# Performance work log

Hardware: AMD Instinct MI355X
Metric: run time of the kernel (lower is better)

## Reference

```python
import jax, jax.numpy as jnp
from jax import lax
import numpy as np

DIM = 8
C = 192
N = 198  # 2 special tokens + 14*14 patches (distilled=True)
B = 1024


def quick_gelu(x):
    return x * jax.nn.sigmoid(1.702 * x)


def setup_inputs() -> dict:
    key = jax.random.key(0)
    ks = jax.random.split(key, 7)
    return {
        "x": jax.random.normal(ks[0], (B, N, C), dtype=jnp.float32),
        "w_down": jax.random.normal(ks[1], (DIM, C), dtype=jnp.float32) * 0.05,
        "b_down": jnp.zeros((DIM,), dtype=jnp.float32),
        "conv_w": jax.random.normal(ks[2], (DIM, DIM, 3, 3), dtype=jnp.float32) * 0.05,
        "conv_b": jnp.zeros((DIM,), dtype=jnp.float32),
        "w_up": jax.random.normal(ks[3], (C, DIM), dtype=jnp.float32) * 0.05,
        "b_up": jnp.zeros((C,), dtype=jnp.float32),
    }


def _conv3x3(t, conv_w, conv_b):
    # t: [B, dim, H, W]; 3x3, stride 1, pad 1 (SAME)
    y = lax.conv_general_dilated(
        t, conv_w, window_strides=(1, 1), padding=((1, 1), (1, 1)),
        dimension_numbers=("NCHW", "OIHW", "NCHW"))
    return y + conv_b[None, :, None, None]


def reference(x, w_down, b_down, conv_w, conv_b, w_up, b_up):
    b, n, c = x.shape
    dim = w_down.shape[0]
    # down projection + QuickGELU
    d = quick_gelu(jnp.einsum("bnc,dc->bnd", x, w_down) + b_down)
    # patch tokens -> [B, dim, 14, 14] -> conv -> [B, 196, dim]
    x_patch = d[:, 2:].reshape(b, 14, 14, dim).transpose(0, 3, 1, 2)
    x_patch = _conv3x3(x_patch, conv_w, conv_b)
    x_patch = x_patch.transpose(0, 2, 3, 1).reshape(b, 14 * 14, dim)
    # cls token -> [B, dim, 1, 1] -> conv (only center tap contributes) -> [B, 1, dim]
    x_cls = d[:, :1].reshape(b, 1, 1, dim).transpose(0, 3, 1, 2)
    x_cls = _conv3x3(x_cls, conv_w, conv_b)
    x_cls = x_cls.transpose(0, 2, 3, 1).reshape(b, 1, dim)
    zero_dist = jnp.zeros_like(x_cls)
    d2 = jnp.concatenate([x_cls, zero_dist, x_patch], axis=1)
    d2 = quick_gelu(d2)  # dropout is identity in eval mode
    return jnp.einsum("bnd,cd->bnc", d2, w_up) + b_up
```

## Files before the change

### kernel.cpp

```cpp
#include <hip/hip_runtime.h>
#include <math.h>

#define NTOK 198
#define CCH  192
#define DIMV 8

typedef float vf4 __attribute__((ext_vector_type(4)));

__device__ __forceinline__ float qgelu(float v) {
    return v / (1.0f + __expf(-1.702f * v));
}

__global__ __launch_bounds__(512, 2) void convpass_fused(
    const float* __restrict__ x,
    const float* __restrict__ w_down,
    const float* __restrict__ b_down,
    const float* __restrict__ conv_w,
    const float* __restrict__ conv_b,
    const float* __restrict__ w_up,
    const float* __restrict__ b_up,
    float* __restrict__ out)
{
    const int b   = blockIdx.x;
    const int tid = threadIdx.x;

    __shared__ float s_w[8 * CCH];
    __shared__ float s_d[NTOK * 9];
    __shared__ float s_d2[NTOK * 8];
    __shared__ float s_cw[576];
    __shared__ float s_cb[8];

    for (int t = tid; t < 8 * CCH; t += 512) s_w[t] = w_down[t];
    for (int t = tid; t < 576; t += 512) {
        const int kk = t >> 6, rem = t & 63, i = rem >> 3, o = rem & 7;
        s_cw[t] = conv_w[(o * 8 + i) * 9 + kk];
    }
    if (tid < 8) s_cb[tid] = conv_b[tid];
    __syncthreads();

    {
        const int lane  = tid & 63;
        const int wv    = tid >> 6;
        const int t_sub = lane >> 3;
        const int k     = lane & 7;
        const float bd  = b_down[k];
        const float* xb = x + (size_t)b * NTOK * CCH;

        #pragma unroll 1
        for (int p = 0; p < 4; ++p) {
            const int n = p * 64 + wv * 8 + t_sub;
            const bool valid = (n < NTOK);
            const int nn = valid ? n : (NTOK - 1);
            const float* xr = xb + (size_t)nn * CCH + k * 24;

            float4 xa[6];
            #pragma unroll
            for (int j = 0; j < 6; ++j) xa[j] = *(const float4*)(xr + 4 * j);

            float acc[8] = {0,0,0,0,0,0,0,0};
            #pragma unroll
            for (int j = 0; j < 6; ++j) {
                #pragma unroll
                for (int dm = 0; dm < 8; ++dm) {
                    const float4 wv4 = *(const float4*)&s_w[dm * CCH + k * 24 + j * 4];
                    acc[dm] += xa[j].x * wv4.x + xa[j].y * wv4.y
                             + xa[j].z * wv4.z + xa[j].w * wv4.w;
                }
            }
            float outv = 0.f;
            #pragma unroll
            for (int dm = 0; dm < 8; ++dm) {
                float v = acc[dm];
                v += __shfl_xor(v, 1); v += __shfl_xor(v, 2); v += __shfl_xor(v, 4);
                outv = (dm == k) ? v : outv;
            }
            if (valid) s_d[n * 9 + k] = qgelu(outv + bd);
        }
    }
    __syncthreads();

    for (int j = tid; j < NTOK * 8; j += 512) {
        const int n = j >> 3, o = j & 7;
        if (n == 1) {
            s_d2[j] = 0.0f;
        } else if (n == 0) {
            float acc = s_cb[o];
            #pragma unroll
            for (int i = 0; i < 8; ++i)
                acc += s_d[i] * s_cw[4 * 64 + i * 8 + o];
            s_d2[j] = qgelu(acc);
        } else {
            const int pos = n - 2, h = pos / 14, w = pos % 14;
            float acc = s_cb[o];
            #pragma unroll
            for (int dh = -1; dh <= 1; ++dh) {
                const int hh = h + dh;
                if (hh < 0 || hh > 13) continue;
                #pragma unroll
                for (int dw = -1; dw <= 1; ++dw) {
                    const int ww = w + dw;
                    if (ww < 0 || ww > 13) continue;
                    const int tok = 2 + hh * 14 + ww;
                    const int kk  = (dh + 1) * 3 + (dw + 1);
                    #pragma unroll
                    for (int i = 0; i < 8; ++i)
                        acc += s_d[tok * 9 + i] * s_cw[kk * 64 + i * 8 + o];
                }
            }
            s_d2[j] = qgelu(acc);
        }
    }

    const int c4 = tid % 48;
    const int tl = tid / 48;
    float w_r[4][8];
    #pragma unroll
    for (int cc = 0; cc < 4; ++cc) {
        const float4 wa = *(const float4*)(w_up + (c4 * 4 + cc) * 8);
        const float4 wb = *(const float4*)(w_up + (c4 * 4 + cc) * 8 + 4);
        w_r[cc][0] = wa.x; w_r[cc][1] = wa.y; w_r[cc][2] = wa.z; w_r[cc][3] = wa.w;
        w_r[cc][4] = wb.x; w_r[cc][5] = wb.y; w_r[cc][6] = wb.z; w_r[cc][7] = wb.w;
    }
    const float4 bu = *(const float4*)(b_up + c4 * 4);
    __syncthreads();

    if (tl < 10) {
        float* outb = out + (size_t)b * NTOK * CCH;
        #pragma unroll 1
        for (int nr = tl; nr < NTOK; nr += 10) {
            const float4 da = *(const float4*)&s_d2[nr * 8];
            const float4 dv = *(const float4*)&s_d2[nr * 8 + 4];
            float accs[4] = {bu.x, bu.y, bu.z, bu.w};
            #pragma unroll
            for (int cc = 0; cc < 4; ++cc) {
                accs[cc] += da.x * w_r[cc][0] + da.y * w_r[cc][1]
                          + da.z * w_r[cc][2] + da.w * w_r[cc][3]
                          + dv.x * w_r[cc][4] + dv.y * w_r[cc][5]
                          + dv.z * w_r[cc][6] + dv.w * w_r[cc][7];
            }
            const vf4 r = {accs[0], accs[1], accs[2], accs[3]};
            __builtin_nontemporal_store(r, (vf4*)(outb + (size_t)nr * CCH + c4 * 4));
        }
    }
}

extern "C" void kernel_launch(void* const* d_in, const int* in_sizes, int n_in,
                              void* d_out, int out_size, void* d_ws, size_t ws_size,
                              hipStream_t stream) {
    const float* x      = (const float*)d_in[0];
    const float* w_down = (const float*)d_in[1];
    const float* b_down = (const float*)d_in[2];
    const float* conv_w = (const float*)d_in[3];
    const float* conv_b = (const float*)d_in[4];
    const float* w_up   = (const float*)d_in[5];
    const float* b_up   = (const float*)d_in[6];
    float* out = (float*)d_out;

    const int B = in_sizes[0] / (NTOK * CCH);
    convpass_fused<<<dim3(B), dim3(512), 0, stream>>>(
        x, w_down, b_down, conv_w, conv_b, w_up, b_up, out);
}
```

Before: 86.11 us.

## Double-buffer x row loads and use a recursive-halving shuffle reduction

```diff
diff --git a/kernel.cpp b/kernel.cpp
--- a/kernel.cpp
+++ b/kernel.cpp
@@ -45,18 +45,14 @@
         const int k     = lane & 7;
         const float bd  = b_down[k];
         const float* xb = x + (size_t)b * NTOK * CCH;
+        const int base  = wv * 8 + t_sub;
 
-        #pragma unroll 1
-        for (int p = 0; p < 4; ++p) {
-            const int n = p * 64 + wv * 8 + t_sub;
-            const bool valid = (n < NTOK);
-            const int nn = valid ? n : (NTOK - 1);
-            const float* xr = xb + (size_t)nn * CCH + k * 24;
+        auto rowp = [&](int n) {
+            const int nn = (n < NTOK) ? n : (NTOK - 1);
+            return xb + (size_t)nn * CCH + k * 24;
+        };
 
-            float4 xa[6];
-            #pragma unroll
-            for (int j = 0; j < 6; ++j) xa[j] = *(const float4*)(xr + 4 * j);
-
+        auto compute = [&](const float4* xa, int n) {
             float acc[8] = {0,0,0,0,0,0,0,0};
             #pragma unroll
             for (int j = 0; j < 6; ++j) {
@@ -67,15 +63,51 @@
                              + xa[j].z * wv4.z + xa[j].w * wv4.w;
                 }
             }
-            float outv = 0.f;
+            float r4[4];
             #pragma unroll
-            for (int dm = 0; dm < 8; ++dm) {
-                float v = acc[dm];
-                v += __shfl_xor(v, 1); v += __shfl_xor(v, 2); v += __shfl_xor(v, 4);
-                outv = (dm == k) ? v : outv;
+            for (int m = 0; m < 4; ++m) {
+                const float give = (k & 1) ? acc[2*m]     : acc[2*m + 1];
+                const float keep = (k & 1) ? acc[2*m + 1] : acc[2*m];
+                r4[m] = keep + __shfl_xor(give, 1);
             }
-            if (valid) s_d[n * 9 + k] = qgelu(outv + bd);
+            float r2[2];
+            #pragma unroll
+            for (int m = 0; m < 2; ++m) {
+                const float give = (k & 2) ? r4[2*m]     : r4[2*m + 1];
+                const float keep = (k & 2) ? r4[2*m + 1] : r4[2*m];
+                r2[m] = keep + __shfl_xor(give, 2);
+            }
+            const float give = (k & 4) ? r2[0] : r2[1];
+            const float keep = (k & 4) ? r2[1] : r2[0];
+            const float v = keep + __shfl_xor(give, 4);
+            if (n < NTOK) s_d[n * 9 + k] = qgelu(v + bd);
+        };
+
+        float4 bufA[6], bufB[6];
+        {
+            const float* p = rowp(base);
+            #pragma unroll
+            for (int j = 0; j < 6; ++j) bufA[j] = *(const float4*)(p + 4 * j);
         }
+        {
+            const float* p = rowp(base + 64);
+            #pragma unroll
+            for (int j = 0; j < 6; ++j) bufB[j] = *(const float4*)(p + 4 * j);
+        }
+        compute(bufA, base);
+        {
+            const float* p = rowp(base + 128);
+            #pragma unroll
+            for (int j = 0; j < 6; ++j) bufA[j] = *(const float4*)(p + 4 * j);
+        }
+        compute(bufB, base + 64);
+        {
+            const float* p = rowp(base + 192);
+            #pragma unroll
+            for (int j = 0; j < 6; ++j) bufB[j] = *(const float4*)(p + 4 * j);
+        }
+        compute(bufA, base + 128);
+        compute(bufB, base + 192);
     }
     __syncthreads();
 
```

New measurement: 104.5 us. 21.4% more time.

## Split each batch's tokens across two 256-thread blocks with halo recompute

Applied to the files above, without the earlier changes.

```diff
diff --git a/kernel.cpp b/kernel.cpp
--- a/kernel.cpp
+++ b/kernel.cpp
@@ -11,7 +11,7 @@
     return v / (1.0f + __expf(-1.702f * v));
 }
 
-__global__ __launch_bounds__(512, 2) void convpass_fused(
+__global__ __launch_bounds__(256, 4) void convpass_fused(
     const float* __restrict__ x,
     const float* __restrict__ w_down,
     const float* __restrict__ b_down,
@@ -21,17 +21,23 @@
     const float* __restrict__ b_up,
     float* __restrict__ out)
 {
-    const int b   = blockIdx.x;
-    const int tid = threadIdx.x;
+    const int half = blockIdx.x;
+    const int b    = blockIdx.y;
+    const int tid  = threadIdx.x;
+
+    const int d_start   = half ? 86  : 0;
+    const int d_count   = half ? 112 : 114;
+    const int out_start = half ? 100 : 0;
+    const int out_count = half ? 98  : 100;
 
     __shared__ float s_w[8 * CCH];
-    __shared__ float s_d[NTOK * 9];
-    __shared__ float s_d2[NTOK * 8];
+    __shared__ float s_d[114 * 9];
+    __shared__ float s_d2[100 * 8];
     __shared__ float s_cw[576];
     __shared__ float s_cb[8];
 
-    for (int t = tid; t < 8 * CCH; t += 512) s_w[t] = w_down[t];
-    for (int t = tid; t < 576; t += 512) {
+    for (int t = tid; t < 8 * CCH; t += 256) s_w[t] = w_down[t];
+    for (int t = tid; t < 576; t += 256) {
         const int kk = t >> 6, rem = t & 63, i = rem >> 3, o = rem & 7;
         s_cw[t] = conv_w[(o * 8 + i) * 9 + kk];
     }
@@ -48,10 +54,10 @@
 
         #pragma unroll 1
         for (int p = 0; p < 4; ++p) {
-            const int n = p * 64 + wv * 8 + t_sub;
-            const bool valid = (n < NTOK);
-            const int nn = valid ? n : (NTOK - 1);
-            const float* xr = xb + (size_t)nn * CCH + k * 24;
+            const int idx = p * 32 + wv * 8 + t_sub;
+            const bool valid = (idx < d_count);
+            const int n = d_start + (valid ? idx : 0);
+            const float* xr = xb + (size_t)n * CCH + k * 24;
 
             float4 xa[6];
             #pragma unroll
@@ -74,13 +80,14 @@
                 v += __shfl_xor(v, 1); v += __shfl_xor(v, 2); v += __shfl_xor(v, 4);
                 outv = (dm == k) ? v : outv;
             }
-            if (valid) s_d[n * 9 + k] = qgelu(outv + bd);
+            if (valid) s_d[idx * 9 + k] = qgelu(outv + bd);
         }
     }
     __syncthreads();
 
-    for (int j = tid; j < NTOK * 8; j += 512) {
-        const int n = j >> 3, o = j & 7;
+    for (int j = tid; j < out_count * 8; j += 256) {
+        const int nr = j >> 3, o = j & 7;
+        const int n = out_start + nr;
         if (n == 1) {
             s_d2[j] = 0.0f;
         } else if (n == 0) {
@@ -102,9 +109,10 @@
                     if (ww < 0 || ww > 13) continue;
                     const int tok = 2 + hh * 14 + ww;
                     const int kk  = (dh + 1) * 3 + (dw + 1);
+                    const int ti  = tok - d_start;
                     #pragma unroll
                     for (int i = 0; i < 8; ++i)
-                        acc += s_d[tok * 9 + i] * s_cw[kk * 64 + i * 8 + o];
+                        acc += s_d[ti * 9 + i] * s_cw[kk * 64 + i * 8 + o];
                 }
             }
             s_d2[j] = qgelu(acc);
@@ -124,10 +132,10 @@
     const float4 bu = *(const float4*)(b_up + c4 * 4);
     __syncthreads();
 
-    if (tl < 10) {
-        float* outb = out + (size_t)b * NTOK * CCH;
+    if (tl < 5) {
+        float* outb = out + ((size_t)b * NTOK + out_start) * CCH;
         #pragma unroll 1
-        for (int nr = tl; nr < NTOK; nr += 10) {
+        for (int nr = tl; nr < out_count; nr += 5) {
             const float4 da = *(const float4*)&s_d2[nr * 8];
             const float4 dv = *(const float4*)&s_d2[nr * 8 + 4];
             float accs[4] = {bu.x, bu.y, bu.z, bu.w};
@@ -157,6 +165,6 @@
     float* out = (float*)d_out;
 
     const int B = in_sizes[0] / (NTOK * CCH);
-    convpass_fused<<<dim3(B), dim3(512), 0, stream>>>(
+    convpass_fused<<<dim3(2, B), dim3(256), 0, stream>>>(
         x, w_down, b_down, conv_w, conv_b, w_up, b_up, out);
 }
```

After: 226.5 us. +163.1%, slower.
